# Performance work log

Measured on AMD Instinct MI355X. Metric: run time of the kernel, lower is better.

## Reference

```python
import jax, jax.numpy as jnp
import numpy as np

B, S, HID, HEADS = 1, 2048, 4096, 32
HEAD_D = HID // HEADS
SCALE = float(1.0 / np.sqrt(HEAD_D))  # = 1/norm_factor^2 with use_mup=False


def setup_inputs() -> dict:
    key = jax.random.key(0)
    k0, k1, k2, k3, k4 = jax.random.split(key, 5)
    return {
        "x": jax.random.normal(k0, (B, S, HID), jnp.float32),
        "attn_qkvw": jax.random.normal(k1, (HID, 3 * HID), jnp.float32) * 0.02,
        "attn_qkvb": jax.random.normal(k2, (3 * HID,), jnp.float32) * 0.02,
        "attn_ow": jax.random.normal(k3, (HID, HID), jnp.float32) * 0.02,
        "attn_ob": jax.random.normal(k4, (HID,), jnp.float32) * 0.02,
    }


def reference(x, attn_qkvw, attn_qkvb, attn_ow, attn_ob):
    # QKV projection (LinearOp): [B,S,HID] @ [HID,3*HID] + bias -> packed qkv
    qkv = x @ attn_qkvw + attn_qkvb
    q, k, v = jnp.split(qkv, 3, axis=-1)  # each [B,S,HID]

    def to_heads(t):
        return t.reshape(B, S, HEADS, HEAD_D)

    q, k, v = to_heads(q), to_heads(k), to_heads(v)
    # flash kernel math: softmax(scale * q k^T + causal mask) @ v (numerically
    # stable online softmax == standard stable softmax)
    scores = jnp.einsum("bqhd,bkhd->bhqk", q, k) * jnp.float32(SCALE)
    causal = jnp.tril(jnp.ones((S, S), dtype=bool))  # P_SEQ = 0
    scores = jnp.where(causal[None, None], scores, jnp.float32(-jnp.inf))
    attn = jax.nn.softmax(scores, axis=-1)
    ctx = jnp.einsum("bhqk,bkhd->bqhd", attn, v).reshape(B, S, HID)
    # output projection
    return ctx @ attn_ow + attn_ob
```

## Files before the change

### kernel.cpp

```cpp
#include <hip/hip_runtime.h>
#include <hip/hip_bf16.h>
#include <math.h>

typedef __bf16 bf16_t;
typedef __bf16 bf16x8 __attribute__((ext_vector_type(8)));
typedef float f32x4 __attribute__((ext_vector_type(4)));

#define AS1 __attribute__((address_space(1)))
#define AS3 __attribute__((address_space(3)))

static constexpr int S_  = 2048;
static constexpr int HID = 4096;
static constexpr int NH  = 32;
static constexpr int HD  = 128;
static constexpr int N3  = 3 * HID;
static constexpr float SCALE = 0.08838834764831845f;

__global__ void cvt_f32_bf16(const float* __restrict__ in, bf16_t* __restrict__ out, int n4) {
  int i = blockIdx.x * blockDim.x + threadIdx.x;
  if (i >= n4) return;
  float4 v = ((const float4*)in)[i];
  union { bf16_t h[4]; short4 s4; } u;
  u.h[0] = (bf16_t)v.x; u.h[1] = (bf16_t)v.y; u.h[2] = (bf16_t)v.z; u.h[3] = (bf16_t)v.w;
  ((short4*)out)[i] = u.s4;
}

__global__ __launch_bounds__(256) void transcvt64(
    const float* __restrict__ in, bf16_t* __restrict__ out, int R, int C) {
  __shared__ float t[64][65];
  const int r0 = blockIdx.y * 64, c0 = blockIdx.x * 64;
  const int tid = threadIdx.x;
  const int rr = tid >> 4, c4 = (tid & 15) * 4;
#pragma unroll
  for (int it = 0; it < 4; ++it) {
    float4 v = *(const float4*)&in[(size_t)(r0 + rr + it * 16) * C + c0 + c4];
    t[rr + it * 16][c4 + 0] = v.x;
    t[rr + it * 16][c4 + 1] = v.y;
    t[rr + it * 16][c4 + 2] = v.z;
    t[rr + it * 16][c4 + 3] = v.w;
  }
  __syncthreads();
  const int cc = tid >> 3, r8 = (tid & 7) * 8;
#pragma unroll
  for (int it = 0; it < 2; ++it) {
    const int c = cc + it * 32;
    bf16x8 w;
#pragma unroll
    for (int j = 0; j < 8; ++j) w[j] = (bf16_t)t[r8 + j][c];
    *(bf16x8*)&out[(size_t)(c0 + c) * R + r0 + r8] = w;
  }
}

__global__ void vtrans(const bf16_t* __restrict__ qkv, bf16_t* __restrict__ vt) {
  __shared__ bf16_t t[32][33];
  int h = blockIdx.z;
  int s0 = blockIdx.x * 32, d0 = blockIdx.y * 32;
  int tx = threadIdx.x, ty = threadIdx.y;
#pragma unroll
  for (int i = 0; i < 32; i += 8)
    t[ty + i][tx] = qkv[(size_t)(s0 + ty + i) * N3 + 2 * HID + h * HD + d0 + tx];
  __syncthreads();
#pragma unroll
  for (int i = 0; i < 32; i += 8)
    vt[(size_t)(h * HD + d0 + ty + i) * S_ + s0 + tx] = t[tx][ty + i];
}

template <bool STG, int VMC>
__device__ __forceinline__ void tile_step(
    const char* slot, int aoff, int boff,
    const bf16_t* gA, const bf16_t* gB, int kst, size_t skA,
    char* stg_dst, f32x4 (&acc)[4][4]) {
  bf16x8 a[4], b[4];
#pragma unroll
  for (int mi = 0; mi < 4; ++mi) a[mi] = *(const bf16x8*)(slot + aoff + mi * 1024);
#pragma unroll
  for (int ni = 0; ni < 4; ++ni) b[ni] = *(const bf16x8*)(slot + 16384 + boff + ni * 1024);
  if constexpr (STG) {
    __builtin_amdgcn_global_load_lds((const AS1 void*)(gA + kst), (AS3 void*)(stg_dst), 16, 0, 0);
    __builtin_amdgcn_global_load_lds((const AS1 void*)(gA + skA + kst), (AS3 void*)(stg_dst + 8192), 16, 0, 0);
    __builtin_amdgcn_global_load_lds((const AS1 void*)(gB + kst), (AS3 void*)(stg_dst + 16384), 16, 0, 0);
  }
  if constexpr (VMC == 3) asm volatile("s_waitcnt vmcnt(3)" ::: "memory");
  else if constexpr (VMC == 0) asm volatile("s_waitcnt vmcnt(0)" ::: "memory");
  __builtin_amdgcn_s_barrier();
  __builtin_amdgcn_s_setprio(1);
#pragma unroll
  for (int mi = 0; mi < 4; ++mi)
#pragma unroll
    for (int ni = 0; ni < 4; ++ni)
      acc[mi][ni] = __builtin_amdgcn_mfma_f32_16x16x32_bf16(a[mi], b[ni], acc[mi][ni], 0, 0, 0);
  __builtin_amdgcn_s_setprio(0);
  __builtin_amdgcn_s_barrier();
}

template <typename OutT>
__global__ __launch_bounds__(512, 4) void gemm_p(
    const bf16_t* __restrict__ A, const bf16_t* __restrict__ BT,
    const float* __restrict__ bias, OutT* __restrict__ C,
    int M, int N, int K, int ntiles) {
  extern __shared__ char smem[];
  const int tid = threadIdx.x;
  const int wv = tid >> 6, ln = tid & 63;
  const int lr = ln & 15, lg = ln >> 4;
  const int wm = wv >> 1, wn = wv & 1;

  const int nx = N >> 7;
  const int chunk = ntiles >> 3;

  const int lrow = wv * 16 + (ln >> 2);
  const int lcol = ((ln & 3) << 3) ^ ((ln & 32) >> 1);
  const size_t skA = (size_t)128 * K;
  const int sw = (lr & 8) << 2;
  const int aoff = (wm * 64 + lr) * 64 + ((lg * 16) ^ sw);
  const int boff = (wn * 64 + lr) * 64 + ((lg * 16) ^ sw);
  const int NT = K >> 5;

  for (int tt = blockIdx.x; tt < ntiles; tt += gridDim.x) {
    const int wg = (tt & 7) * chunk + (tt >> 3);
    const int m0 = (wg / nx) * 256, n0 = (wg % nx) * 128;

    const bf16_t* gA = A + (size_t)(m0 + lrow) * K + lcol;
    const bf16_t* gB = BT + (size_t)(n0 + lrow) * K + lcol;

    f32x4 acc[4][4] = {};

#pragma unroll
    for (int t = 0; t < 2; ++t) {
      char* d = smem + t * 24576 + wv * 1024;
      __builtin_amdgcn_global_load_lds((const AS1 void*)(gA + t * 32), (AS3 void*)(d), 16, 0, 0);
      __builtin_amdgcn_global_load_lds((const AS1 void*)(gA + skA + t * 32), (AS3 void*)(d + 8192), 16, 0, 0);
      __builtin_amdgcn_global_load_lds((const AS1 void*)(gB + t * 32), (AS3 void*)(d + 16384), 16, 0, 0);
    }
    asm volatile("s_waitcnt vmcnt(3)" ::: "memory");
    __builtin_amdgcn_s_barrier();

    int slot = 0, nslot = 2;
    int t = 0;
    for (; t < NT - 2; ++t) {
      tile_step<true, 3>(smem + slot * 24576, aoff, boff, gA, gB, (t + 2) * 32,
                         skA, smem + nslot * 24576 + wv * 1024, acc);
      slot = (slot == 2) ? 0 : slot + 1;
      nslot = (nslot == 2) ? 0 : nslot + 1;
    }
    tile_step<false, 0>(smem + slot * 24576, aoff, boff, gA, gB, 0, skA, smem, acc);
    slot = (slot == 2) ? 0 : slot + 1;
    tile_step<false, -1>(smem + slot * 24576, aoff, boff, gA, gB, 0, skA, smem, acc);

#pragma unroll
    for (int mi = 0; mi < 4; ++mi)
#pragma unroll
      for (int ni = 0; ni < 4; ++ni) {
        const int col = n0 + wn * 64 + ni * 16 + lr;
        const float bv = bias[col];
#pragma unroll
        for (int i = 0; i < 4; ++i) {
          const int row = m0 + wm * 64 + mi * 16 + lg * 4 + i;
          C[(size_t)row * N + col] = (OutT)(acc[mi][ni][i] + bv);
        }
      }
  }
}

__global__ __launch_bounds__(256, 2) void attn_fwd(
    const bf16_t* __restrict__ qkv, const bf16_t* __restrict__ vt,
    bf16_t* __restrict__ ctx) {
  __shared__ __align__(16) bf16_t Ks[64][136];
  __shared__ __align__(16) bf16_t Vts[128][72];

  const int tid = threadIdx.x;
  const int wv = tid >> 6, ln = tid & 63;
  bf16_t* Pl = &Ks[0][0] + wv * (32 * 68);

  const int bid = blockIdx.x;
  const int a = bid >> 3;
  const int hsub = a >> 4;
  const int h  = ((bid & 7) << 2) + hsub;
  const int qt = 15 - (((a & 15) + (hsub << 2)) & 15);
  const int q0 = qt * 128;
  const int lr = ln & 15, lg = ln >> 4;
  const int rbase = q0 + 32 * wv;

  bf16x8 qf[2][4];
#pragma unroll
  for (int rg = 0; rg < 2; ++rg)
#pragma unroll
    for (int kk = 0; kk < 4; ++kk) {
      bf16x8 r = *(const bf16x8*)(qkv + (size_t)(rbase + 16 * rg + lr) * N3 + h * HD + kk * 32 + lg * 8);
#pragma unroll
      for (int j = 0; j < 8; ++j) r[j] = (bf16_t)((float)r[j] * SCALE);
      qf[rg][kk] = r;
    }

  f32x4 oacc[2][8] = {};
  float mrow[2][4], psum[2][4];
#pragma unroll
  for (int rg = 0; rg < 2; ++rg)
#pragma unroll
    for (int i = 0; i < 4; ++i) { mrow[rg][i] = -INFINITY; psum[rg][i] = 0.f; }

  const int ntiles = 2 * qt + 2;
  for (int t = 0; t < ntiles; ++t) {
    const int kv0 = t * 64;
    __syncthreads();
#pragma unroll
    for (int it = 0; it < 4; ++it) {
      int c = tid + it * 256;
      {
        int row = c >> 4, col = (c & 15) * 8;
        *(bf16x8*)&Ks[row][col] =
            *(const bf16x8*)(qkv + (size_t)(kv0 + row) * N3 + HID + h * HD + col);
      }
      {
        int row = c >> 3, col = (c & 7) * 8;
        *(bf16x8*)&Vts[row][col] =
            *(const bf16x8*)(vt + (size_t)(h * HD + row) * S_ + kv0 + col);
      }
    }
    __syncthreads();

    f32x4 sacc[2][4] = {};
#pragma unroll
    for (int kk = 0; kk < 4; ++kk)
#pragma unroll
      for (int ni = 0; ni < 4; ++ni) {
        bf16x8 kf = *(const bf16x8*)&Ks[16 * ni + lr][kk * 32 + lg * 8];
        sacc[0][ni] = __builtin_amdgcn_mfma_f32_16x16x32_bf16(qf[0][kk], kf, sacc[0][ni], 0, 0, 0);
        sacc[1][ni] = __builtin_amdgcn_mfma_f32_16x16x32_bf16(qf[1][kk], kf, sacc[1][ni], 0, 0, 0);
      }

    float p[2][4][4];
    float mx[2][4];
    bool grow = false;
#pragma unroll
    for (int rg = 0; rg < 2; ++rg) {
      const bool needmask = (kv0 + 63 > rbase + 16 * rg);
#pragma unroll
      for (int i = 0; i < 4; ++i) {
        const int row = rbase + 16 * rg + lg * 4 + i;
        float m_ = -INFINITY;
#pragma unroll
        for (int ni = 0; ni < 4; ++ni) {
          float s = sacc[rg][ni][i];
          if (needmask && (kv0 + 16 * ni + lr > row)) s = -INFINITY;
          p[rg][ni][i] = s;
          m_ = fmaxf(m_, s);
        }
        m_ = fmaxf(m_, __shfl_xor(m_, 1, 64));
        m_ = fmaxf(m_, __shfl_xor(m_, 2, 64));
        m_ = fmaxf(m_, __shfl_xor(m_, 4, 64));
        m_ = fmaxf(m_, __shfl_xor(m_, 8, 64));
        mx[rg][i] = m_;
        grow |= (m_ > mrow[rg][i]);
      }
    }
    if (__any(grow)) {
#pragma unroll
      for (int rg = 0; rg < 2; ++rg) {
        float alpha[4];
#pragma unroll
        for (int i = 0; i < 4; ++i) {
          const float mn = fmaxf(mrow[rg][i], mx[rg][i]);
          alpha[i] = __expf(mrow[rg][i] - mn);
          mrow[rg][i] = mn;
          psum[rg][i] *= alpha[i];
        }
#pragma unroll
        for (int nf = 0; nf < 8; ++nf)
#pragma unroll
          for (int i = 0; i < 4; ++i) oacc[rg][nf][i] *= alpha[i];
      }
    }
#pragma unroll
    for (int rg = 0; rg < 2; ++rg)
#pragma unroll
      for (int i = 0; i < 4; ++i) {
        float ps = 0.f;
#pragma unroll
        for (int ni = 0; ni < 4; ++ni) {
          float e = __expf(p[rg][ni][i] - mrow[rg][i]);
          p[rg][ni][i] = e;
          ps += e;
        }
        psum[rg][i] += ps;
      }

    __syncthreads();

#pragma unroll
    for (int rg = 0; rg < 2; ++rg)
#pragma unroll
      for (int ni = 0; ni < 4; ++ni)
#pragma unroll
        for (int i = 0; i < 4; ++i)
          Pl[(16 * rg + lg * 4 + i) * 68 + 16 * ni + lr] = (bf16_t)p[rg][ni][i];

#pragma unroll
    for (int kk2 = 0; kk2 < 2; ++kk2) {
      bf16x8 pf0 = *(const bf16x8*)&Pl[lr * 68 + kk2 * 32 + lg * 8];
      bf16x8 pf1 = *(const bf16x8*)&Pl[(16 + lr) * 68 + kk2 * 32 + lg * 8];
#pragma unroll
      for (int nf = 0; nf < 8; ++nf) {
        bf16x8 vf = *(const bf16x8*)&Vts[16 * nf + lr][kk2 * 32 + lg * 8];
        oacc[0][nf] = __builtin_amdgcn_mfma_f32_16x16x32_bf16(pf0, vf, oacc[0][nf], 0, 0, 0);
        oacc[1][nf] = __builtin_amdgcn_mfma_f32_16x16x32_bf16(pf1, vf, oacc[1][nf], 0, 0, 0);
      }
    }
  }

#pragma unroll
  for (int rg = 0; rg < 2; ++rg) {
#pragma unroll
    for (int i = 0; i < 4; ++i) {
      float s = psum[rg][i];
      s += __shfl_xor(s, 1, 64);
      s += __shfl_xor(s, 2, 64);
      s += __shfl_xor(s, 4, 64);
      s += __shfl_xor(s, 8, 64);
      psum[rg][i] = 1.f / s;
    }
#pragma unroll
    for (int nf = 0; nf < 8; ++nf)
#pragma unroll
      for (int i = 0; i < 4; ++i) {
        int row = rbase + 16 * rg + lg * 4 + i;
        int col = h * HD + 16 * nf + lr;
        ctx[(size_t)row * HID + col] = (bf16_t)(oacc[rg][nf][i] * psum[rg][i]);
      }
  }
}

extern "C" void kernel_launch(void* const* d_in, const int* in_sizes, int n_in,
                              void* d_out, int out_size, void* d_ws, size_t ws_size,
                              hipStream_t stream) {
  const float* x    = (const float*)d_in[0];
  const float* wqkv = (const float*)d_in[1];
  const float* bqkv = (const float*)d_in[2];
  const float* ow   = (const float*)d_in[3];
  const float* ob   = (const float*)d_in[4];
  float* out = (float*)d_out;

  char* w = (char*)d_ws;
  bf16_t* xb    = (bf16_t*)(w);
  bf16_t* wqkvT = (bf16_t*)(w + (size_t)16777216);
  bf16_t* qkv   = (bf16_t*)(w + (size_t)117440512);
  bf16_t* vt    = (bf16_t*)(w + (size_t)167772160);
  bf16_t* ctx   = (bf16_t*)(w + (size_t)184549376);
  bf16_t* owT   = (bf16_t*)(w + (size_t)201326592);

  (void)in_sizes; (void)n_in; (void)out_size; (void)ws_size;

  cvt_f32_bf16<<<(S_ * HID / 4 + 255) / 256, 256, 0, stream>>>(x, xb, S_ * HID / 4);
  transcvt64<<<dim3(N3 / 64, HID / 64), 256, 0, stream>>>(wqkv, wqkvT, HID, N3);
  transcvt64<<<dim3(HID / 64, HID / 64), 256, 0, stream>>>(ow, owT, HID, HID);
  gemm_p<bf16_t><<<512, 512, 73728, stream>>>(xb, wqkvT, bqkv, qkv, S_, N3, HID,
                                              (S_ / 256) * (N3 / 128));
  vtrans<<<dim3(S_ / 32, HD / 32, NH), dim3(32, 8), 0, stream>>>(qkv, vt);
  attn_fwd<<<(S_ / 128) * NH, 256, 0, stream>>>(qkv, vt, ctx);
  gemm_p<float><<<256, 512, 73728, stream>>>(ctx, owT, ob, out, S_, HID, HID,
                                             (S_ / 256) * (HID / 128));
}
```

Before: 510.3 us.

## Use 4-wave GEMM with larger per-wave tiles for QKV projection

Adds a new QKV projection GEMM kernel that uses 256 threads (4 waves) per block instead of 512. Each wave computes a 128x64 sub-tile with 8x4 MFMA accumulators. The three-slot LDS pipeline with global_load_lds staging is kept, and launch bounds are set to 2 blocks per CU. The aim is more register-level reuse of A/B fragments per MFMA and lower barrier/sync overhead, at the cost of higher register pressure and fewer waves to hide latency.

```diff
diff --git a/kernel.cpp b/kernel.cpp
--- a/kernel.cpp
+++ b/kernel.cpp
@@ -63,6 +63,113 @@
 #pragma unroll
   for (int i = 0; i < 32; i += 8)
     vt[(size_t)(h * HD + d0 + ty + i) * S_ + s0 + tx] = t[tx][ty + i];
+}
+
+template <bool STG, int VMC>
+__device__ __forceinline__ void wstep(
+    const char* slot, int aoff, int boff,
+    const bf16_t* gA, const bf16_t* gB, int kst, size_t row64,
+    char* stgA, char* stgB, f32x4 (&acc)[8][4]) {
+  bf16x8 a[8], b[4];
+#pragma unroll
+  for (int mi = 0; mi < 8; ++mi) a[mi] = *(const bf16x8*)(slot + aoff + mi * 1024);
+#pragma unroll
+  for (int ni = 0; ni < 4; ++ni) b[ni] = *(const bf16x8*)(slot + 16384 + boff + ni * 1024);
+  if constexpr (STG) {
+#pragma unroll
+    for (int i = 0; i < 4; ++i)
+      __builtin_amdgcn_global_load_lds((const AS1 void*)(gA + i * row64 + kst),
+                                       (AS3 void*)(stgA + i * 4096), 16, 0, 0);
+#pragma unroll
+    for (int j = 0; j < 2; ++j)
+      __builtin_amdgcn_global_load_lds((const AS1 void*)(gB + j * row64 + kst),
+                                       (AS3 void*)(stgB + j * 4096), 16, 0, 0);
+  }
+  if constexpr (VMC == 6) asm volatile("s_waitcnt vmcnt(6)" ::: "memory");
+  else if constexpr (VMC == 0) asm volatile("s_waitcnt vmcnt(0)" ::: "memory");
+  __builtin_amdgcn_s_barrier();
+  __builtin_amdgcn_s_setprio(1);
+#pragma unroll
+  for (int mi = 0; mi < 8; ++mi)
+#pragma unroll
+    for (int ni = 0; ni < 4; ++ni)
+      acc[mi][ni] = __builtin_amdgcn_mfma_f32_16x16x32_bf16(a[mi], b[ni], acc[mi][ni], 0, 0, 0);
+  __builtin_amdgcn_s_setprio(0);
+  __builtin_amdgcn_s_barrier();
+}
+
+__global__ __launch_bounds__(256, 2) void gemm_w(
+    const bf16_t* __restrict__ A, const bf16_t* __restrict__ BT,
+    const float* __restrict__ bias, bf16_t* __restrict__ C,
+    int M, int N, int K, int ntiles) {
+  extern __shared__ char smem[];
+  const int tid = threadIdx.x;
+  const int wv = tid >> 6, ln = tid & 63;
+  const int lr = ln & 15, lg = ln >> 4;
+  const int wm = wv >> 1, wn = wv & 1;
+
+  const int nx = N >> 7;
+  const int chunk = ntiles >> 3;
+
+  const int lrow = wv * 16 + (ln >> 2);
+  const int lcol = ((ln & 3) << 3) ^ ((ln & 32) >> 1);
+  const size_t row64 = (size_t)64 * K;
+  const int sw = (lr & 8) << 2;
+  const int aoff = (wm * 128 + lr) * 64 + ((lg * 16) ^ sw);
+  const int boff = (wn * 64 + lr) * 64 + ((lg * 16) ^ sw);
+  const int NT = K >> 5;
+
+  for (int tt = blockIdx.x; tt < ntiles; tt += gridDim.x) {
+    const int wg = (tt & 7) * chunk + (tt >> 3);
+    const int m0 = (wg / nx) * 256, n0 = (wg % nx) * 128;
+
+    const bf16_t* gA = A + (size_t)(m0 + lrow) * K + lcol;
+    const bf16_t* gB = BT + (size_t)(n0 + lrow) * K + lcol;
+
+    f32x4 acc[8][4] = {};
+
+#pragma unroll
+    for (int t = 0; t < 2; ++t) {
+      char* dA = smem + t * 24576 + wv * 1024;
+      char* dB = dA + 16384;
+#pragma unroll
+      for (int i = 0; i < 4; ++i)
+        __builtin_amdgcn_global_load_lds((const AS1 void*)(gA + i * row64 + t * 32),
+                                         (AS3 void*)(dA + i * 4096), 16, 0, 0);
+#pragma unroll
+      for (int j = 0; j < 2; ++j)
+        __builtin_amdgcn_global_load_lds((const AS1 void*)(gB + j * row64 + t * 32),
+                                         (AS3 void*)(dB + j * 4096), 16, 0, 0);
+    }
+    asm volatile("s_waitcnt vmcnt(6)" ::: "memory");
+    __builtin_amdgcn_s_barrier();
+
+    int slot = 0, nslot = 2;
+    int t = 0;
+    for (; t < NT - 2; ++t) {
+      char* sb = smem + nslot * 24576 + wv * 1024;
+      wstep<true, 6>(smem + slot * 24576, aoff, boff, gA, gB, (t + 2) * 32,
+                     row64, sb, sb + 16384, acc);
+      slot = (slot == 2) ? 0 : slot + 1;
+      nslot = (nslot == 2) ? 0 : nslot + 1;
+    }
+    wstep<false, 0>(smem + slot * 24576, aoff, boff, gA, gB, 0, row64, smem, smem, acc);
+    slot = (slot == 2) ? 0 : slot + 1;
+    wstep<false, -1>(smem + slot * 24576, aoff, boff, gA, gB, 0, row64, smem, smem, acc);
+
+#pragma unroll
+    for (int mi = 0; mi < 8; ++mi)
+#pragma unroll
+      for (int ni = 0; ni < 4; ++ni) {
+        const int col = n0 + wn * 64 + ni * 16 + lr;
+        const float bv = bias[col];
+#pragma unroll
+        for (int i = 0; i < 4; ++i) {
+          const int row = m0 + wm * 128 + mi * 16 + lg * 4 + i;
+          C[(size_t)row * N + col] = (bf16_t)(acc[mi][ni][i] + bv);
+        }
+      }
+  }
 }
 
 template <bool STG, int VMC>
@@ -352,8 +459,8 @@
   cvt_f32_bf16<<<(S_ * HID / 4 + 255) / 256, 256, 0, stream>>>(x, xb, S_ * HID / 4);
   transcvt64<<<dim3(N3 / 64, HID / 64), 256, 0, stream>>>(wqkv, wqkvT, HID, N3);
   transcvt64<<<dim3(HID / 64, HID / 64), 256, 0, stream>>>(ow, owT, HID, HID);
-  gemm_p<bf16_t><<<512, 512, 73728, stream>>>(xb, wqkvT, bqkv, qkv, S_, N3, HID,
-                                              (S_ / 256) * (N3 / 128));
+  gemm_w<<<512, 256, 73728, stream>>>(xb, wqkvT, bqkv, qkv, S_, N3, HID,
+                                      (S_ / 256) * (N3 / 128));
   vtrans<<<dim3(S_ / 32, HD / 32, NH), dim3(32, 8), 0, stream>>>(qkv, vt);
   attn_fwd<<<(S_ / 128) * NH, 256, 0, stream>>>(qkv, vt, ctx);
   gemm_p<float><<<256, 512, 73728, stream>>>(ctx, owT, ob, out, S_, HID, HID,
```

New measurement: 508.2 us. No clear change (-0.4%).

## Rewrite GEMM as 8-wave ping-pong pipeline and prefetch attention K/V tiles

Applied to the files above, without the earlier changes.

Replaces the GEMM main loop with an 8-wave kernel. Each block computes a 128x256 tile with a K-step of 64, double-buffered in 96KB of LDS. The loop is split into four MFMA quadrants, with global_load_lds staging and swizzled LDS reads interleaved between barriers, so memory traffic overlaps compute. The attention kernel now prefetches the next K/V tile into registers while the current tile is stored to shared memory. This adds register pressure and more barriers, and lowers occupancy from 4 to 2 blocks per CU.

```diff
diff --git a/kernel.cpp b/kernel.cpp
--- a/kernel.cpp
+++ b/kernel.cpp
@@ -65,36 +65,8 @@
     vt[(size_t)(h * HD + d0 + ty + i) * S_ + s0 + tx] = t[tx][ty + i];
 }
 
-template <bool STG, int VMC>
-__device__ __forceinline__ void tile_step(
-    const char* slot, int aoff, int boff,
-    const bf16_t* gA, const bf16_t* gB, int kst, size_t skA,
-    char* stg_dst, f32x4 (&acc)[4][4]) {
-  bf16x8 a[4], b[4];
-#pragma unroll
-  for (int mi = 0; mi < 4; ++mi) a[mi] = *(const bf16x8*)(slot + aoff + mi * 1024);
-#pragma unroll
-  for (int ni = 0; ni < 4; ++ni) b[ni] = *(const bf16x8*)(slot + 16384 + boff + ni * 1024);
-  if constexpr (STG) {
-    __builtin_amdgcn_global_load_lds((const AS1 void*)(gA + kst), (AS3 void*)(stg_dst), 16, 0, 0);
-    __builtin_amdgcn_global_load_lds((const AS1 void*)(gA + skA + kst), (AS3 void*)(stg_dst + 8192), 16, 0, 0);
-    __builtin_amdgcn_global_load_lds((const AS1 void*)(gB + kst), (AS3 void*)(stg_dst + 16384), 16, 0, 0);
-  }
-  if constexpr (VMC == 3) asm volatile("s_waitcnt vmcnt(3)" ::: "memory");
-  else if constexpr (VMC == 0) asm volatile("s_waitcnt vmcnt(0)" ::: "memory");
-  __builtin_amdgcn_s_barrier();
-  __builtin_amdgcn_s_setprio(1);
-#pragma unroll
-  for (int mi = 0; mi < 4; ++mi)
-#pragma unroll
-    for (int ni = 0; ni < 4; ++ni)
-      acc[mi][ni] = __builtin_amdgcn_mfma_f32_16x16x32_bf16(a[mi], b[ni], acc[mi][ni], 0, 0, 0);
-  __builtin_amdgcn_s_setprio(0);
-  __builtin_amdgcn_s_barrier();
-}
-
 template <typename OutT>
-__global__ __launch_bounds__(512, 4) void gemm_p(
+__global__ __launch_bounds__(512, 2) void gemm8p(
     const bf16_t* __restrict__ A, const bf16_t* __restrict__ BT,
     const float* __restrict__ bias, OutT* __restrict__ C,
     int M, int N, int K, int ntiles) {
@@ -102,49 +74,129 @@
   const int tid = threadIdx.x;
   const int wv = tid >> 6, ln = tid & 63;
   const int lr = ln & 15, lg = ln >> 4;
-  const int wm = wv >> 1, wn = wv & 1;
-
-  const int nx = N >> 7;
+  const int wm = wv >> 2, wn = wv & 3;
+  const int nx = N >> 8;
   const int chunk = ntiles >> 3;
-
-  const int lrow = wv * 16 + (ln >> 2);
-  const int lcol = ((ln & 3) << 3) ^ ((ln & 32) >> 1);
-  const size_t skA = (size_t)128 * K;
-  const int sw = (lr & 8) << 2;
-  const int aoff = (wm * 64 + lr) * 64 + ((lg * 16) ^ sw);
-  const int boff = (wn * 64 + lr) * 64 + ((lg * 16) ^ sw);
-  const int NT = K >> 5;
+  (void)M;
+
+  const int srow = ln >> 3;
+  const int scol = 8 * ((ln & 7) ^ srow);
+  const int xorb = (lr & 7) << 4;
+  const int NI = K >> 7;
 
   for (int tt = blockIdx.x; tt < ntiles; tt += gridDim.x) {
     const int wg = (tt & 7) * chunk + (tt >> 3);
-    const int m0 = (wg / nx) * 256, n0 = (wg % nx) * 128;
-
-    const bf16_t* gA = A + (size_t)(m0 + lrow) * K + lcol;
-    const bf16_t* gB = BT + (size_t)(n0 + lrow) * K + lcol;
+    const int m0 = (wg / nx) * 128, n0 = (wg % nx) * 256;
+
+    const bf16_t* gA = A + (size_t)(m0 + wv * 16 + srow) * K + scol;
+    const bf16_t* gB = BT + (size_t)(n0 + wv * 32 + srow) * K + scol;
+
+    auto STG = [&](int l, int t, int c) {
+      if (l < 2) {
+        __builtin_amdgcn_global_load_lds(
+            (const AS1 void*)(gA + (size_t)l * 8 * K + t * 64),
+            (AS3 void*)(smem + c * 49152 + wv * 2048 + l * 1024 + ln * 16), 16, 0, 0);
+      } else {
+        const int jl = l - 2;
+        __builtin_amdgcn_global_load_lds(
+            (const AS1 void*)(gB + (size_t)jl * 8 * K + t * 64),
+            (AS3 void*)(smem + c * 49152 + 16384 + wv * 4096 + jl * 1024 + ln * 16), 16, 0, 0);
+      }
+    };
+    auto LDA = [&](int c, int mi, int kk) {
+      return *(const bf16x8*)(smem + c * 49152 + (wm * 64 + mi * 16 + lr) * 128 +
+                              ((kk * 64 + lg * 16) ^ xorb));
+    };
+    auto LDB = [&](int c, int ni, int kk) {
+      return *(const bf16x8*)(smem + c * 49152 + 16384 + (wn * 64 + ni * 16 + lr) * 128 +
+                              ((kk * 64 + lg * 16) ^ xorb));
+    };
 
     f32x4 acc[4][4] = {};
 
 #pragma unroll
-    for (int t = 0; t < 2; ++t) {
-      char* d = smem + t * 24576 + wv * 1024;
-      __builtin_amdgcn_global_load_lds((const AS1 void*)(gA + t * 32), (AS3 void*)(d), 16, 0, 0);
-      __builtin_amdgcn_global_load_lds((const AS1 void*)(gA + skA + t * 32), (AS3 void*)(d + 8192), 16, 0, 0);
-      __builtin_amdgcn_global_load_lds((const AS1 void*)(gB + t * 32), (AS3 void*)(d + 16384), 16, 0, 0);
-    }
-    asm volatile("s_waitcnt vmcnt(3)" ::: "memory");
-    __builtin_amdgcn_s_barrier();
-
-    int slot = 0, nslot = 2;
-    int t = 0;
-    for (; t < NT - 2; ++t) {
-      tile_step<true, 3>(smem + slot * 24576, aoff, boff, gA, gB, (t + 2) * 32,
-                         skA, smem + nslot * 24576 + wv * 1024, acc);
-      slot = (slot == 2) ? 0 : slot + 1;
-      nslot = (nslot == 2) ? 0 : nslot + 1;
-    }
-    tile_step<false, 0>(smem + slot * 24576, aoff, boff, gA, gB, 0, skA, smem, acc);
-    slot = (slot == 2) ? 0 : slot + 1;
-    tile_step<false, -1>(smem + slot * 24576, aoff, boff, gA, gB, 0, skA, smem, acc);
+    for (int l = 0; l < 6; ++l) STG(l, 0, 0);
+#pragma unroll
+    for (int l = 0; l < 6; ++l) STG(l, 1, 1);
+
+#define QUAD(MI0, NI0)                                                              \
+  __builtin_amdgcn_s_setprio(1);                                                    \
+  _Pragma("unroll") for (int mi = MI0; mi < MI0 + 2; ++mi)                          \
+  _Pragma("unroll") for (int ni = NI0; ni < NI0 + 2; ++ni)                          \
+  _Pragma("unroll") for (int kk = 0; kk < 2; ++kk)                                  \
+      acc[mi][ni] = __builtin_amdgcn_mfma_f32_16x16x32_bf16(a[mi][kk], b[ni][kk],   \
+                                                            acc[mi][ni], 0, 0, 0);  \
+  __builtin_amdgcn_s_setprio(0);
+#define BARRIER() __builtin_amdgcn_s_barrier(); __builtin_amdgcn_sched_barrier(0)
+#define LGKM0() asm volatile("s_waitcnt lgkmcnt(0)" ::: "memory"); __builtin_amdgcn_sched_barrier(0)
+
+    for (int j = 0; j < NI; ++j) {
+      const int tB = 2 * j + 1;
+      const bool e = (j != 0);
+      const bool md = (j != NI - 1);
+      bf16x8 a[4][2], b[4][2];
+
+      if (e) { STG(2, tB, 1); STG(3, tB, 1); }
+      asm volatile("s_waitcnt vmcnt(4)" ::: "memory");
+      BARRIER();
+#pragma unroll
+      for (int mi = 0; mi < 2; ++mi) { a[mi][0] = LDA(0, mi, 0); a[mi][1] = LDA(0, mi, 1); }
+#pragma unroll
+      for (int ni = 0; ni < 2; ++ni) { b[ni][0] = LDB(0, ni, 0); b[ni][1] = LDB(0, ni, 1); }
+      LGKM0();
+      QUAD(0, 0);
+      BARRIER();
+      if (e) STG(4, tB, 1);
+#pragma unroll
+      for (int ni = 2; ni < 4; ++ni) { b[ni][0] = LDB(0, ni, 0); b[ni][1] = LDB(0, ni, 1); }
+      BARRIER();
+      LGKM0();
+      QUAD(0, 2);
+      BARRIER();
+      if (e) STG(5, tB, 1);
+#pragma unroll
+      for (int mi = 2; mi < 4; ++mi) { a[mi][0] = LDA(0, mi, 0); a[mi][1] = LDA(0, mi, 1); }
+      BARRIER();
+      LGKM0();
+      QUAD(2, 0);
+      BARRIER();
+      if (md) { STG(0, 2 * j + 2, 0); STG(1, 2 * j + 2, 0); }
+      BARRIER();
+      QUAD(2, 2);
+      BARRIER();
+      if (md) { STG(2, 2 * j + 2, 0); STG(3, 2 * j + 2, 0); }
+      if (md) { asm volatile("s_waitcnt vmcnt(4)" ::: "memory"); }
+      else    { asm volatile("s_waitcnt vmcnt(0)" ::: "memory"); }
+      BARRIER();
+#pragma unroll
+      for (int mi = 0; mi < 2; ++mi) { a[mi][0] = LDA(1, mi, 0); a[mi][1] = LDA(1, mi, 1); }
+#pragma unroll
+      for (int ni = 0; ni < 2; ++ni) { b[ni][0] = LDB(1, ni, 0); b[ni][1] = LDB(1, ni, 1); }
+      LGKM0();
+      QUAD(0, 0);
+      BARRIER();
+      if (md) STG(4, 2 * j + 2, 0);
+#pragma unroll
+      for (int ni = 2; ni < 4; ++ni) { b[ni][0] = LDB(1, ni, 0); b[ni][1] = LDB(1, ni, 1); }
+      BARRIER();
+      LGKM0();
+      QUAD(0, 2);
+      BARRIER();
+      if (md) STG(5, 2 * j + 2, 0);
+#pragma unroll
+      for (int mi = 2; mi < 4; ++mi) { a[mi][0] = LDA(1, mi, 0); a[mi][1] = LDA(1, mi, 1); }
+      BARRIER();
+      LGKM0();
+      QUAD(2, 0);
+      BARRIER();
+      if (md) { STG(0, 2 * j + 3, 1); STG(1, 2 * j + 3, 1); }
+      BARRIER();
+      QUAD(2, 2);
+      BARRIER();
+    }
+#undef QUAD
+#undef BARRIER
+#undef LGKM0
 
 #pragma unroll
     for (int mi = 0; mi < 4; ++mi)
@@ -198,23 +250,30 @@
 #pragma unroll
     for (int i = 0; i < 4; ++i) { mrow[rg][i] = -INFINITY; psum[rg][i] = 0.f; }
 
+  const int k_r = tid >> 4, k_c = (tid & 15) * 8;
+  const int v_r = tid >> 3, v_c = (tid & 7) * 8;
+  bf16x8 kr[4], vr[4];
+
+#pragma unroll
+  for (int it = 0; it < 4; ++it) {
+    kr[it] = *(const bf16x8*)(qkv + (size_t)(k_r + it * 16) * N3 + HID + h * HD + k_c);
+    vr[it] = *(const bf16x8*)(vt + (size_t)(h * HD + v_r + it * 32) * S_ + v_c);
+  }
+
   const int ntiles = 2 * qt + 2;
   for (int t = 0; t < ntiles; ++t) {
     const int kv0 = t * 64;
+    const int kvn = (t + 1 < ntiles) ? kv0 + 64 : 0;
     __syncthreads();
 #pragma unroll
     for (int it = 0; it < 4; ++it) {
-      int c = tid + it * 256;
-      {
-        int row = c >> 4, col = (c & 15) * 8;
-        *(bf16x8*)&Ks[row][col] =
-            *(const bf16x8*)(qkv + (size_t)(kv0 + row) * N3 + HID + h * HD + col);
-      }
-      {
-        int row = c >> 3, col = (c & 7) * 8;
-        *(bf16x8*)&Vts[row][col] =
-            *(const bf16x8*)(vt + (size_t)(h * HD + row) * S_ + kv0 + col);
-      }
+      *(bf16x8*)&Ks[k_r + it * 16][k_c] = kr[it];
+      *(bf16x8*)&Vts[v_r + it * 32][v_c] = vr[it];
+    }
+#pragma unroll
+    for (int it = 0; it < 4; ++it) {
+      kr[it] = *(const bf16x8*)(qkv + (size_t)(kvn + k_r + it * 16) * N3 + HID + h * HD + k_c);
+      vr[it] = *(const bf16x8*)(vt + (size_t)(h * HD + v_r + it * 32) * S_ + kvn + v_c);
     }
     __syncthreads();
 
@@ -352,10 +411,10 @@
   cvt_f32_bf16<<<(S_ * HID / 4 + 255) / 256, 256, 0, stream>>>(x, xb, S_ * HID / 4);
   transcvt64<<<dim3(N3 / 64, HID / 64), 256, 0, stream>>>(wqkv, wqkvT, HID, N3);
   transcvt64<<<dim3(HID / 64, HID / 64), 256, 0, stream>>>(ow, owT, HID, HID);
-  gemm_p<bf16_t><<<512, 512, 73728, stream>>>(xb, wqkvT, bqkv, qkv, S_, N3, HID,
-                                              (S_ / 256) * (N3 / 128));
+  gemm8p<bf16_t><<<256, 512, 98304, stream>>>(xb, wqkvT, bqkv, qkv, S_, N3, HID,
+                                              (S_ / 128) * (N3 / 256));
   vtrans<<<dim3(S_ / 32, HD / 32, NH), dim3(32, 8), 0, stream>>>(qkv, vt);
   attn_fwd<<<(S_ / 128) * NH, 256, 0, stream>>>(qkv, vt, ctx);
-  gemm_p<float><<<256, 512, 73728, stream>>>(ctx, owT, ob, out, S_, HID, HID,
-                                             (S_ / 256) * (HID / 128));
-}
+  gemm8p<float><<<256, 512, 98304, stream>>>(ctx, owT, ob, out, S_, HID, HID,
+                                             (S_ / 128) * (HID / 256));
+}
```

Measured after the change: 515.5 us. About the same (+1.0%).
